# Performance work log

Hardware: AMD Instinct MI355X
Metric: run time of the kernel (lower is better)

Reference implementation:

```python
import jax, jax.numpy as jnp
import numpy as np

N = 13627
E = 504378
D = 500


def _seg_softmax(e, seg, n):
    m = jax.ops.segment_max(e, seg, num_segments=n)
    ex = jnp.exp(e - m[seg])
    s = jax.ops.segment_sum(ex, seg, num_segments=n)
    return ex / (s[seg] + 1e-16)


def _gatv2(x, src, dst, Wl, Wr, att, b, n):
    # PyG GATv2Conv (heads=1): message = Wl x_src; score uses Wl x_src + Wr x_dst
    xl = x @ Wl                                   # [N, F]
    xr = x @ Wr                                   # [N, F]
    e = jax.nn.leaky_relu(xl[src] + xr[dst], 0.2) @ att   # [E]
    a = _seg_softmax(e, dst, n)                   # segment softmax over targets
    out = jax.ops.segment_sum(a[:, None] * xl[src], dst, num_segments=n)
    return out + b


def setup_inputs() -> dict:
    key = jax.random.key(0)
    ks = jax.random.split(key, 24)
    s = 0.05
    inp = {
        'x': jax.random.normal(ks[0], (N, D), dtype=jnp.float32),
        'edge_index': jax.random.randint(ks[1], (2, E), 0, N),
        'neg_edge_index': jax.random.randint(ks[2], (2, E), 0, N),
        'Wl1': jax.random.normal(ks[3], (D, 300)) * s,
        'Wr1': jax.random.normal(ks[4], (D, 300)) * s,
        'att1': jax.random.normal(ks[5], (300,)) * s,
        'b1': jnp.zeros((300,)),
        'Wl2': jax.random.normal(ks[6], (300, 100)) * s,
        'Wr2': jax.random.normal(ks[7], (300, 100)) * s,
        'att2': jax.random.normal(ks[8], (100,)) * s,
        'b2': jnp.zeros((100,)),
        'Wl3': jax.random.normal(ks[9], (100, 1)) * s,
        'Wr3': jax.random.normal(ks[10], (100, 1)) * s,
        'att3': jax.random.normal(ks[11], (1,)) * s,
        'b3': jnp.zeros((1,)),
        'W_lin1': jax.random.normal(ks[12], (D, 100)) * s,
        'b_lin1': jnp.zeros((100,)),
        'W_lin2': jax.random.normal(ks[13], (D, 100)) * s,
        'b_lin2': jnp.zeros((100,)),
        'c1': jnp.array([0.5], dtype=jnp.float32),
        'c2': jnp.array([0.5], dtype=jnp.float32),
    }
    return inp


def reference(x, edge_index, neg_edge_index, Wl1, Wr1, att1, b1, Wl2, Wr2, att2, b2,
              Wl3, Wr3, att3, b3, W_lin1, b_lin1, W_lin2, b_lin2, c1, c2):
    # eval mode: dropout / dropout_adj are identity
    loops = jnp.arange(N)
    src = jnp.concatenate([edge_index[0], loops])   # GATv2Conv adds self loops
    dst = jnp.concatenate([edge_index[1], loops])

    h1 = jax.nn.relu(_gatv2(x, src, dst, Wl1, Wr1, att1, b1, N))
    h2 = jax.nn.relu(_gatv2(h1, src, dst, Wl2, Wr2, att2, b2, N))

    xo = h2 + jax.nn.relu(x @ W_lin1 + b_lin1)
    z = h2 + jax.nn.relu(x @ W_lin2 + b_lin2)

    # link-prediction reconstruction loss
    pos_s = jnp.sum(z[edge_index[0]] * z[edge_index[1]], axis=1)
    pos_loss = -jnp.mean(jnp.log(jax.nn.sigmoid(pos_s) + 1e-15))
    neg_s = jnp.sum(z[neg_edge_index[0]] * z[neg_edge_index[1]], axis=1)
    neg_loss = -jnp.mean(jnp.log(1.0 - jax.nn.sigmoid(neg_s) + 1e-15))
    r_loss = pos_loss + neg_loss

    out = _gatv2(xo, src, dst, Wl3, Wr3, att3, b3, N)   # [N, 1]
    return out, r_loss, c1, c2
```

## Files before the change

### kernel.cpp

```cpp
#include <hip/hip_runtime.h>
#include <hip/hip_bf16.h>

#define NODES 13627
#define DIM   500

typedef short short8 __attribute__((ext_vector_type(8)));
typedef float f32x4 __attribute__((ext_vector_type(4)));
typedef float floatx2 __attribute__((ext_vector_type(2)));

__device__ inline float wave_reduce_sum(float v) {
#pragma unroll
    for (int o = 32; o > 0; o >>= 1) v += __shfl_xor(v, o, 64);
    return v;
}

__device__ inline void store_v(float* p, float v) { *p = v; }
__device__ inline void store_v(__hip_bfloat16* p, float v) { *p = __float2bfloat16(v); }

__device__ inline float blo(unsigned w) { unsigned t = w << 16;        return __builtin_bit_cast(float, t); }
__device__ inline float bhi(unsigned w) { unsigned t = w & 0xffff0000u; return __builtin_bit_cast(float, t); }

__device__ inline unsigned char to_fp8(float v) {
    int r = __builtin_amdgcn_cvt_pk_fp8_f32(v, v, 0, false);
    return (unsigned char)(r & 0xff);
}

__device__ inline unsigned pk2bf(float a, float b) {
    unsigned la = (unsigned)__builtin_bit_cast(unsigned short, __float2bfloat16(a));
    unsigned hb = (unsigned)__builtin_bit_cast(unsigned short, __float2bfloat16(b));
    return la | (hb << 16);
}

struct b4 { __hip_bfloat16 a, b, c, d; };

__global__ __launch_bounds__(256) void hist_kernel(const int* __restrict__ dst,
                                                   int* __restrict__ cnt, int E) {
    int i = blockIdx.x * blockDim.x + threadIdx.x;
    if (i < E) atomicAdd(&cnt[dst[i]], 1);
}

__global__ __launch_bounds__(1024) void scan_kernel(int* __restrict__ cnt_cur,
                                                    int* __restrict__ off, int n) {
    __shared__ int wsum[16];
    const int tid = threadIdx.x, lane = tid & 63, w = tid >> 6;
    int carry = 0;
    for (int base = 0; base < n; base += 1024) {
        int i = base + tid;
        int v = (i < n) ? cnt_cur[i] : 0;
        int s = v;
#pragma unroll
        for (int o = 1; o < 64; o <<= 1) {
            int t = __shfl_up(s, o, 64);
            if (lane >= o) s += t;
        }
        if (lane == 63) wsum[w] = s;
        __syncthreads();
        if (w == 0 && lane < 16) {
            int x = wsum[lane];
            int sx = x;
#pragma unroll
            for (int o = 1; o < 16; o <<= 1) {
                int t = __shfl_up(sx, o, 64);
                if (lane >= o) sx += t;
            }
            wsum[lane] = sx;
        }
        __syncthreads();
        int wo = (w == 0) ? 0 : wsum[w - 1];
        int total = wsum[15];
        int excl = carry + wo + (s - v);
        if (i < n) { off[i] = excl; cnt_cur[i] = excl; }
        carry += total;
        __syncthreads();
    }
    if (tid == 0) off[n] = carry;
}

__global__ __launch_bounds__(256) void scatter_kernel(const int* __restrict__ src,
                                                      const int* __restrict__ dst,
                                                      int* __restrict__ cur,
                                                      int* __restrict__ ssrc, int E) {
    int i = blockIdx.x * blockDim.x + threadIdx.x;
    if (i < E) {
        int p = atomicAdd(&cur[dst[i]], 1);
        ssrc[p] = src[i];
    }
}

__global__ __launch_bounds__(256) void convert_all_kernel(
    const float* __restrict__ x,
    const float* __restrict__ Wl1, const float* __restrict__ Wr1,
    const float* __restrict__ Wl2, const float* __restrict__ Wr2,
    const float* __restrict__ Ws1, const float* __restrict__ Ws2,
    const float* __restrict__ bs1, const float* __restrict__ bs2,
    __hip_bfloat16* __restrict__ W1T, __hip_bfloat16* __restrict__ W2T,
    __hip_bfloat16* __restrict__ WsT, float* __restrict__ bcat,
    __hip_bfloat16* __restrict__ xb, int M) {
    int i = blockIdx.x * 256 + threadIdx.x;
    if (i < 327680) {
        int n = i >> 9, k = i & 511;
        float v = 0.f;
        if (k < 500) {
            if (n < 300) v = Wl1[k * 300 + n];
            else if (n < 600) v = Wr1[k * 300 + n - 300];
        }
        W1T[i] = __float2bfloat16(v);
    } else if (i < 409600) {
        int j = i - 327680;
        int n = j / 320, k = j - n * 320;
        float v = 0.f;
        if (k < 300) {
            if (n < 100) v = Wl2[k * 100 + n];
            else if (n < 200) v = Wr2[k * 100 + n - 100];
        }
        W2T[j] = __float2bfloat16(v);
    } else if (i < 540672) {
        int j = i - 409600;
        int n = j >> 9, k = j & 511;
        float v = 0.f;
        if (k < 500) {
            if (n < 100) v = Ws1[k * 100 + n];
            else if (n < 200) v = Ws2[k * 100 + n - 100];
        }
        WsT[j] = __float2bfloat16(v);
    } else if (i < 540928) {
        int n = i - 540672;
        float v = 0.f;
        if (n < 100) v = bs1[n];
        else if (n < 200) v = bs2[n - 100];
        bcat[n] = v;
    } else {
        int j = i - 540928;
        if (j >= M * 128) return;
        int m = j >> 7, k = (j & 127) << 2;
        b4 o;
        if (k < 500) {
            float4 v = *(const float4*)(x + (size_t)m * 500 + k);
            o.a = __float2bfloat16(v.x); o.b = __float2bfloat16(v.y);
            o.c = __float2bfloat16(v.z); o.d = __float2bfloat16(v.w);
        } else {
            o.a = o.b = o.c = o.d = __float2bfloat16(0.f);
        }
        *(b4*)(xb + (size_t)m * 512 + k) = o;
    }
}

template <int EPI, typename TC>
__global__ __launch_bounds__(256) void mfma_gemm(
    const __hip_bfloat16* __restrict__ A, const __hip_bfloat16* __restrict__ BT,
    TC* __restrict__ C, const float* __restrict__ bias, const float* __restrict__ h2,
    unsigned char* __restrict__ p8, __hip_bfloat16* __restrict__ pb,
    int M, int Kp, int Nn, int ldc) {
    __shared__ short AsF[8 * 64 * 8];
    __shared__ short BsF[4 * 64 * 8];
    const int t = threadIdx.x;
    const int w = t >> 6, lane = t & 63;
    const int c = t & 3, rr = t >> 2;
    const int m0 = blockIdx.y * 128, n0 = blockIdx.x * 64;

    f32x4 acc[2][4];
#pragma unroll
    for (int i = 0; i < 2; i++)
#pragma unroll
        for (int j = 0; j < 4; j++) acc[i][j] = (f32x4){0.f, 0.f, 0.f, 0.f};

    for (int k0 = 0; k0 < Kp; k0 += 32) {
#pragma unroll
        for (int r = 0; r < 2; r++) {
            int m = r * 64 + rr;
            int gm = m0 + m; if (gm >= M) gm = M - 1;
            float4 v = *(const float4*)(A + (size_t)gm * Kp + k0 + c * 8);
            int mi = m >> 4, sl = m & 15;
            *(float4*)(&AsF[(mi * 64 + c * 16 + sl) * 8]) = v;
        }
        {
            int n = rr;
            float4 v = *(const float4*)(BT + (size_t)(n0 + n) * Kp + k0 + c * 8);
            int ni = n >> 4, sl = n & 15;
            *(float4*)(&BsF[(ni * 64 + c * 16 + sl) * 8]) = v;
        }
        __syncthreads();
        short8 a0 = *(const short8*)(&AsF[((w * 2 + 0) * 64 + lane) * 8]);
        short8 a1 = *(const short8*)(&AsF[((w * 2 + 1) * 64 + lane) * 8]);
#pragma unroll
        for (int j = 0; j < 4; j++) {
            short8 b = *(const short8*)(&BsF[(j * 64 + lane) * 8]);
            acc[0][j] = __builtin_amdgcn_mfma_f32_16x16x32_bf16(a0, b, acc[0][j], 0, 0, 0);
            acc[1][j] = __builtin_amdgcn_mfma_f32_16x16x32_bf16(a1, b, acc[1][j], 0, 0, 0);
        }
        __syncthreads();
    }

    const int q = lane >> 4, sl = lane & 15;
#pragma unroll
    for (int i = 0; i < 2; i++) {
#pragma unroll
        for (int j = 0; j < 4; j++) {
#pragma unroll
            for (int reg = 0; reg < 4; reg++) {
                int gm = m0 + w * 32 + i * 16 + q * 4 + reg;
                int gn = n0 + j * 16 + sl;
                if (gm >= M) continue;
                float v = acc[i][j][reg];
                if constexpr (EPI == 1) {
                    if (gn < 300)       p8[(size_t)gm * 304 + gn] = to_fp8(v);
                    else if (gn < 600)  pb[(size_t)gm * 320 + (gn - 300)] = __float2bfloat16(v);
                    else if (gn < 620)  pb[(size_t)gm * 320 + (gn - 300)] = __float2bfloat16(0.f);
                    else if (gn < 624)  p8[(size_t)gm * 304 + (gn - 320)] = 0;
                } else if constexpr (EPI == 2) {
                    if (gn < 100)       p8[(size_t)gm * 112 + gn] = to_fp8(v);
                    else if (gn < 200)  pb[(size_t)gm * 128 + (gn - 100)] = __float2bfloat16(v);
                    else if (gn < 212)  p8[(size_t)gm * 112 + (gn - 100)] = 0;
                    else if (gn < 240)  pb[(size_t)gm * 128 + (gn - 112)] = __float2bfloat16(0.f);
                } else if constexpr (EPI == 3) {
                    if (gn < 200) {
                        int cn = gn < 100 ? gn : gn - 100;
                        float val = fmaxf(v + bias[gn], 0.f) + h2[(size_t)gm * 100 + cn];
                        if (gn < 100) C[(size_t)gm * 100 + gn] = val;
                        else p8[(size_t)gm * 128 + (gn - 100)] = to_fp8(val);
                    } else if (gn < 228) {
                        p8[(size_t)gm * 128 + (gn - 100)] = 0;
                    }
                } else {
                    store_v(&C[(size_t)gm * ldc + gn], v);
                }
            }
        }
    }
}

template <int F, int NJ, int SL8, int SRB, int SOUT, int JSL, typename TOUT>
__global__ __launch_bounds__(256) void gat_f8_kernel(
    const unsigned char* __restrict__ xl8, const __hip_bfloat16* __restrict__ xrb,
    const float* __restrict__ att, const float* __restrict__ bias,
    const int* __restrict__ off, const int* __restrict__ ssrc,
    TOUT* __restrict__ out, int n) {
    __shared__ float sden[2];
    __shared__ float sacc[2][NJ * 64];
    const int t = threadIdx.x;
    const int lane = t & 63;
    const int sl = lane & 15, q = lane >> 4;
    const int half = (t >> 6) & 1;
    const int pairIdx = t >> 7;
    int wid = blockIdx.x * 2 + pairIdx;
    if (wid >= n) wid = n - 1;

    float attv[NJ * 4], xrv[NJ * 4], acc[NJ * 4];
    const unsigned* xru = (const unsigned*)xrb + (size_t)wid * (SRB / 2);
#pragma unroll
    for (int j = 0; j < NJ; j++) {
        const int f0 = sl * 4 + j * 64;
        if (f0 < F) {
            float4 a4 = *(const float4*)(att + f0);
            attv[j * 4 + 0] = a4.x; attv[j * 4 + 1] = a4.y;
            attv[j * 4 + 2] = a4.z; attv[j * 4 + 3] = a4.w;
        } else {
            attv[j * 4 + 0] = attv[j * 4 + 1] = attv[j * 4 + 2] = attv[j * 4 + 3] = 0.f;
        }
        unsigned u0 = __builtin_nontemporal_load(xru + (f0 >> 1));
        unsigned u1 = __builtin_nontemporal_load(xru + (f0 >> 1) + 1);
        xrv[j * 4 + 0] = blo(u0); xrv[j * 4 + 1] = bhi(u0);
        xrv[j * 4 + 2] = blo(u1); xrv[j * 4 + 3] = bhi(u1);
        acc[j * 4 + 0] = acc[j * 4 + 1] = acc[j * 4 + 2] = acc[j * 4 + 3] = 0.f;
    }

    const int s0 = off[wid], s1 = off[wid + 1];
    const int h0 = (s1 - s0) >> 1;
    const int eb = half ? (s0 + h0) : (s0 - 1);
    const int ee = half ? s1 : (s0 + h0);
    float den = 0.f;

    unsigned u[NJ];
    {
        int eq = eb + q;
        int src = wid;
        if (eq >= s0 && eq < ee) src = __builtin_nontemporal_load(ssrc + eq);
        const unsigned char* row = xl8 + (size_t)src * SL8;
#pragma unroll
        for (int j = 0; j < NJ; j++) {
            const bool ld = (j < NJ - 1) || (sl < JSL);
            u[j] = ld ? *(const unsigned*)(row + sl * 4 + j * 64) : 0u;
        }
    }

    for (int e0 = eb; e0 < ee; e0 += 4) {
        const bool act = (e0 + q) < ee;
        unsigned un[NJ];
        {
            int eq1 = e0 + 4 + q;
            int src1 = wid;
            if (eq1 >= s0 && eq1 < ee) src1 = __builtin_nontemporal_load(ssrc + eq1);
            const unsigned char* row1 = xl8 + (size_t)src1 * SL8;
#pragma unroll
            for (int j = 0; j < NJ; j++) {
                const bool ld = (j < NJ - 1) || (sl < JSL);
                un[j] = ld ? *(const unsigned*)(row1 + sl * 4 + j * 64) : 0u;
            }
        }
        float xlv[NJ * 4];
        float p = 0.f;
#pragma unroll
        for (int j = 0; j < NJ; j++) {
            floatx2 lo = __builtin_amdgcn_cvt_pk_f32_fp8((int)u[j], false);
            floatx2 hi = __builtin_amdgcn_cvt_pk_f32_fp8((int)u[j], true);
            float v[4] = {lo.x, lo.y, hi.x, hi.y};
#pragma unroll
            for (int cc = 0; cc < 4; cc++) {
                xlv[j * 4 + cc] = v[cc];
                float s = v[cc] + xrv[j * 4 + cc];
                p += attv[j * 4 + cc] * fmaxf(s, 0.2f * s);
            }
        }
        p += __shfl_xor(p, 1, 64);
        p += __shfl_xor(p, 2, 64);
        p += __shfl_xor(p, 4, 64);
        p += __shfl_xor(p, 8, 64);
        float ex = act ? expf(p) : 0.f;
        den += ex;
#pragma unroll
        for (int i = 0; i < NJ * 4; i++) acc[i] += ex * xlv[i];
#pragma unroll
        for (int j = 0; j < NJ; j++) u[j] = un[j];
    }

#pragma unroll
    for (int o = 16; o <= 32; o <<= 1) {
        den += __shfl_xor(den, o, 64);
#pragma unroll
        for (int i = 0; i < NJ * 4; i++) acc[i] += __shfl_xor(acc[i], o, 64);
    }

    if (half == 1 && lane < 16) {
        if (lane == 0) sden[pairIdx] = den;
#pragma unroll
        for (int j = 0; j < NJ; j++)
            *(float4*)(&sacc[pairIdx][sl * 4 + j * 64]) =
                make_float4(acc[j * 4 + 0], acc[j * 4 + 1], acc[j * 4 + 2], acc[j * 4 + 3]);
    }
    __syncthreads();
    if (half == 0 && lane < 16) {
        den += sden[pairIdx];
        const float inv = 1.f / (den + 1e-16f);
#pragma unroll
        for (int j = 0; j < NJ; j++) {
            const int f0 = sl * 4 + j * 64;
            if (f0 >= SOUT) continue;
            float4 o4 = *(float4*)(&sacc[pairIdx][f0]);
            float vv[4] = {acc[j * 4 + 0] + o4.x, acc[j * 4 + 1] + o4.y,
                           acc[j * 4 + 2] + o4.z, acc[j * 4 + 3] + o4.w};
            float r[4];
#pragma unroll
            for (int cc = 0; cc < 4; cc++) {
                const int f = f0 + cc;
                float v = 0.f;
                if (f < F) v = fmaxf(vv[cc] * inv + bias[f], 0.f);
                r[cc] = v;
            }
            if constexpr (sizeof(TOUT) == 4) {
                *(float4*)((float*)out + (size_t)wid * SOUT + f0) =
                    make_float4(r[0], r[1], r[2], r[3]);
            } else {
                unsigned* op = (unsigned*)out + (size_t)wid * (SOUT / 2) + (f0 >> 1);
                op[0] = pk2bf(r[0], r[1]);
                op[1] = pk2bf(r[2], r[3]);
            }
        }
    }
}

__global__ __launch_bounds__(256) void gemm_vec1_kernel(
    const float* __restrict__ xo, const float* __restrict__ wl,
    const float* __restrict__ wr, float* __restrict__ xl3,
    float* __restrict__ xr3, int M, int ldx) {
    const int wid = blockIdx.x * 4 + (threadIdx.x >> 6);
    const int lane = threadIdx.x & 63;
    if (wid >= M) return;
    float a = 0.f, b = 0.f;
    for (int f = lane; f < 100; f += 64) {
        float v = xo[(size_t)wid * ldx + f];
        a += v * wl[f];
        b += v * wr[f];
    }
    a = wave_reduce_sum(a);
    b = wave_reduce_sum(b);
    if (lane == 0) { xl3[wid] = a; xr3[wid] = b; }
}

__global__ __launch_bounds__(256) void gat3_kernel(
    const float* __restrict__ xl3, const float* __restrict__ xr3,
    const float* __restrict__ att3, const float* __restrict__ b3,
    const int* __restrict__ off, const int* __restrict__ ssrc,
    float* __restrict__ out, int n) {
    const int wid = blockIdx.x * 4 + (threadIdx.x >> 6);
    const int lane = threadIdx.x & 63;
    if (wid >= n) return;
    const float xrv = xr3[wid];
    const float att = att3[0];
    float num = 0.f, den = 0.f;
    const int s0 = off[wid], s1 = off[wid + 1];
    for (int e = s0 - 1 + lane; e < s1; e += 64) {
        int src = (e < s0) ? wid : ssrc[e];
        float xlv = xl3[src];
        float t = xlv + xrv;
        float g = t > 0.f ? t : 0.2f * t;
        float ex = expf(g * att);
        den += ex;
        num += ex * xlv;
    }
    num = wave_reduce_sum(num);
    den = wave_reduce_sum(den);
    if (lane == 0) out[wid] = num / (den + 1e-16f) + b3[0];
}

__global__ __launch_bounds__(256) void loss_kernel(
    const unsigned char* __restrict__ z8, const int* __restrict__ pos,
    const int* __restrict__ neg, float* __restrict__ part, int nb, int E) {
    const int lane = threadIdx.x & 63;
    const int sl = lane & 15;
    const int wlocal = threadIdx.x >> 6;
    const int q = lane >> 4;
    const int nq = gridDim.x * 16;
    const int qid = (blockIdx.x * 4 + wlocal) * 4 + q;
    const int total = 2 * E;
    float psum = 0.f, nsum = 0.f;

    for (int base = qid; base < total; base += 4 * nq) {
        uint2 au[4], bu[4];
        bool act[4], isN[4];
#pragma unroll
        for (int s = 0; s < 4; s++) {
            int it = base + s * nq;
            act[s] = it < total;
            int itc = act[s] ? it : 0;
            isN[s] = itc >= E;
            int e = isN[s] ? itc - E : itc;
            const int* ei = isN[s] ? neg : pos;
            int u = ei[e], v = ei[E + e];
            au[s] = *(const uint2*)(z8 + (size_t)u * 128 + sl * 8);
            bu[s] = *(const uint2*)(z8 + (size_t)v * 128 + sl * 8);
        }
#pragma unroll
        for (int s = 0; s < 4; s++) {
            floatx2 a0 = __builtin_amdgcn_cvt_pk_f32_fp8((int)au[s].x, false);
            floatx2 a1 = __builtin_amdgcn_cvt_pk_f32_fp8((int)au[s].x, true);
            floatx2 a2 = __builtin_amdgcn_cvt_pk_f32_fp8((int)au[s].y, false);
            floatx2 a3 = __builtin_amdgcn_cvt_pk_f32_fp8((int)au[s].y, true);
            floatx2 b0 = __builtin_amdgcn_cvt_pk_f32_fp8((int)bu[s].x, false);
            floatx2 b1 = __builtin_amdgcn_cvt_pk_f32_fp8((int)bu[s].x, true);
            floatx2 b2 = __builtin_amdgcn_cvt_pk_f32_fp8((int)bu[s].y, false);
            floatx2 b3 = __builtin_amdgcn_cvt_pk_f32_fp8((int)bu[s].y, true);
            float p = a0.x * b0.x + a0.y * b0.y + a1.x * b1.x + a1.y * b1.y
                    + a2.x * b2.x + a2.y * b2.y + a3.x * b3.x + a3.y * b3.y;
            p += __shfl_xor(p, 1, 64);
            p += __shfl_xor(p, 2, 64);
            p += __shfl_xor(p, 4, 64);
            p += __shfl_xor(p, 8, 64);
            if (sl == 0 && act[s]) {
                float sig = 1.f / (1.f + expf(-p));
                if (isN[s]) nsum += logf(1.f - sig + 1e-15f);
                else        psum += logf(sig + 1e-15f);
            }
        }
    }
    float pw = wave_reduce_sum(psum);
    float nw = wave_reduce_sum(nsum);
    __shared__ float sp[4], sn[4];
    if (lane == 0) { sp[wlocal] = pw; sn[wlocal] = nw; }
    __syncthreads();
    if (threadIdx.x == 0) {
        part[blockIdx.x]      = sp[0] + sp[1] + sp[2] + sp[3];
        part[nb + blockIdx.x] = sn[0] + sn[1] + sn[2] + sn[3];
    }
}

__global__ __launch_bounds__(1024) void finalize_kernel(
    const float* __restrict__ part, int nb,
    const float* __restrict__ c1, const float* __restrict__ c2,
    float* __restrict__ out, int n, int E) {
    __shared__ float sp[16], sn[16];
    const int tid = threadIdx.x, lane = tid & 63, w = tid >> 6;
    float p = 0.f, q = 0.f;
    for (int i = tid; i < nb; i += 1024) { p += part[i]; q += part[nb + i]; }
    p = wave_reduce_sum(p);
    q = wave_reduce_sum(q);
    if (lane == 0) { sp[w] = p; sn[w] = q; }
    __syncthreads();
    if (tid == 0) {
        float tp = 0.f, tq = 0.f;
#pragma unroll
        for (int i = 0; i < 16; i++) { tp += sp[i]; tq += sn[i]; }
        out[n]     = -(tp + tq) / (float)E;
        out[n + 1] = c1[0];
        out[n + 2] = c2[0];
    }
}

extern "C" void kernel_launch(void* const* d_in, const int* in_sizes, int n_in,
                              void* d_out, int out_size, void* d_ws, size_t ws_size,
                              hipStream_t stream) {
    const float* x      = (const float*)d_in[0];
    const int*   ei     = (const int*)d_in[1];
    const int*   nei    = (const int*)d_in[2];
    const float* Wl1    = (const float*)d_in[3];
    const float* Wr1    = (const float*)d_in[4];
    const float* att1   = (const float*)d_in[5];
    const float* b1     = (const float*)d_in[6];
    const float* Wl2    = (const float*)d_in[7];
    const float* Wr2    = (const float*)d_in[8];
    const float* att2   = (const float*)d_in[9];
    const float* b2     = (const float*)d_in[10];
    const float* Wl3    = (const float*)d_in[11];
    const float* Wr3    = (const float*)d_in[12];
    const float* att3   = (const float*)d_in[13];
    const float* b3     = (const float*)d_in[14];
    const float* Wlin1  = (const float*)d_in[15];
    const float* blin1  = (const float*)d_in[16];
    const float* Wlin2  = (const float*)d_in[17];
    const float* blin2  = (const float*)d_in[18];
    const float* c1     = (const float*)d_in[19];
    const float* c2     = (const float*)d_in[20];
    float* out = (float*)d_out;

    const int E = in_sizes[1] / 2;
    const int N = NODES;
    const int LOSS_BLOCKS = 4096;

    char* ws = (char*)d_ws;
    unsigned char*  xl8  = (unsigned char*)(ws + 0);
    unsigned char*  xl28 = (unsigned char*)(ws + 0);
    __hip_bfloat16* xrb  = (__hip_bfloat16*)(ws + 4194304);
    __hip_bfloat16* xr2b = (__hip_bfloat16*)(ws + 4194304);
    float*          xo   = (float*)(ws + 4194304);
    unsigned char*  z8   = (unsigned char*)(ws + 9645312);
    __hip_bfloat16* h1b  = (__hip_bfloat16*)(ws + 12915712);
    float*          h2   = (float*)(ws + 12915712);
    __hip_bfloat16* xb   = (__hip_bfloat16*)(ws + 21637120);
    __hip_bfloat16* W1T  = (__hip_bfloat16*)(ws + 35591168);
    __hip_bfloat16* W2T  = (__hip_bfloat16*)(ws + 36246528);
    __hip_bfloat16* WsT  = (__hip_bfloat16*)(ws + 36410368);
    float*          bcat = (float*)(ws + 36672512);
    float*          xl3  = (float*)(ws + 36673536);
    float*          xr3  = (float*)(ws + 36728064);
    int*            ioff = (int*)(ws + 36782592);
    int*            cur  = (int*)(ws + 36837376);
    int*            ssrc = (int*)(ws + 36892160);
    float*          part = (float*)(ws + 38909952);

    hipMemsetAsync(cur, 0, sizeof(int) * N, stream);

    hist_kernel<<<(E + 255) / 256, 256, 0, stream>>>(ei + E, cur, E);
    scan_kernel<<<1, 1024, 0, stream>>>(cur, ioff, N);
    scatter_kernel<<<(E + 255) / 256, 256, 0, stream>>>(ei, ei + E, cur, ssrc, E);

    convert_all_kernel<<<(540928 + N * 128 + 255) / 256, 256, 0, stream>>>(
        x, Wl1, Wr1, Wl2, Wr2, Wlin1, Wlin2, blin1, blin2,
        W1T, W2T, WsT, bcat, xb, N);

    mfma_gemm<1, __hip_bfloat16><<<dim3(10, 107), 256, 0, stream>>>(
        xb, W1T, (__hip_bfloat16*)nullptr, nullptr, nullptr, xl8, xrb, N, 512, 640, 0);
    gat_f8_kernel<300, 5, 304, 320, 320, 11, __hip_bfloat16>
        <<<(N + 1) / 2, 256, 0, stream>>>(xl8, xrb, att1, b1, ioff, ssrc, h1b, N);

    mfma_gemm<2, __hip_bfloat16><<<dim3(4, 107), 256, 0, stream>>>(
        h1b, W2T, (__hip_bfloat16*)nullptr, nullptr, nullptr, xl28, xr2b, N, 320, 256, 0);
    gat_f8_kernel<100, 2, 112, 128, 100, 9, float>
        <<<(N + 1) / 2, 256, 0, stream>>>(xl28, xr2b, att2, b2, ioff, ssrc, h2, N);

    mfma_gemm<3, float><<<dim3(4, 107), 256, 0, stream>>>(
        xb, WsT, xo, bcat, h2, z8, nullptr, N, 512, 256, 0);

    loss_kernel<<<LOSS_BLOCKS, 256, 0, stream>>>(z8, ei, nei, part, LOSS_BLOCKS, E);

    gemm_vec1_kernel<<<(N + 3) / 4, 256, 0, stream>>>(xo, Wl3, Wr3, xl3, xr3, N, 100);
    gat3_kernel<<<(N + 3) / 4, 256, 0, stream>>>(xl3, xr3, att3, b3, ioff, ssrc, out, N);

    finalize_kernel<<<1, 1024, 0, stream>>>(part, LOSS_BLOCKS, c1, c2, out, N, E);
}
```

Baseline: 390.4 us.

## Split leaky-ReLU into linear plus abs terms, precompute linear part in GEMM epilogue

Rewrites leaky_relu(s) as 0.6*s + 0.4*|s|, so the linear term att·(xl_src + xr_dst) is computed once per node in the GEMM epilogue via shuffle reductions and atomics into per-node scalars. The edge loop then only does an fma with |s| and adds the two precomputed scalars, replacing a max and multiply per feature. In exchange it adds atomics and reductions to the GEMM epilogue, an extra memset, and a per-edge scalar gather. The linear term now comes from fp32 accumulators rather than the fp8-quantized xl values, which slightly changes the numerics.

```diff
diff --git a/kernel.cpp b/kernel.cpp
--- a/kernel.cpp
+++ b/kernel.cpp
@@ -150,6 +150,7 @@
     const __hip_bfloat16* __restrict__ A, const __hip_bfloat16* __restrict__ BT,
     TC* __restrict__ C, const float* __restrict__ bias, const float* __restrict__ h2,
     unsigned char* __restrict__ p8, __hip_bfloat16* __restrict__ pb,
+    const float* __restrict__ attw, float* __restrict__ sxl, float* __restrict__ sxr,
     int M, int Kp, int Nn, int ldc) {
     __shared__ short AsF[8 * 64 * 8];
     __shared__ short BsF[4 * 64 * 8];
@@ -192,37 +193,75 @@
     }
 
     const int q = lane >> 4, sl = lane & 15;
-#pragma unroll
-    for (int i = 0; i < 2; i++) {
-#pragma unroll
-        for (int j = 0; j < 4; j++) {
+    if constexpr (EPI == 1 || EPI == 2) {
+        constexpr int XL_END = (EPI == 1) ? 300 : 100;
+        constexpr int XR_END = 2 * XL_END;
+        constexpr int SL8s   = (EPI == 1) ? 304 : 112;
+        constexpr int SRBs   = (EPI == 1) ? 320 : 128;
+        const bool hasXl = n0 < XL_END;
+        const bool hasXr = (n0 + 63 >= XL_END) && (n0 < XR_END);
+#pragma unroll
+        for (int i = 0; i < 2; i++) {
 #pragma unroll
             for (int reg = 0; reg < 4; reg++) {
                 int gm = m0 + w * 32 + i * 16 + q * 4 + reg;
-                int gn = n0 + j * 16 + sl;
                 if (gm >= M) continue;
-                float v = acc[i][j][reg];
-                if constexpr (EPI == 1) {
-                    if (gn < 300)       p8[(size_t)gm * 304 + gn] = to_fp8(v);
-                    else if (gn < 600)  pb[(size_t)gm * 320 + (gn - 300)] = __float2bfloat16(v);
-                    else if (gn < 620)  pb[(size_t)gm * 320 + (gn - 300)] = __float2bfloat16(0.f);
-                    else if (gn < 624)  p8[(size_t)gm * 304 + (gn - 320)] = 0;
-                } else if constexpr (EPI == 2) {
-                    if (gn < 100)       p8[(size_t)gm * 112 + gn] = to_fp8(v);
-                    else if (gn < 200)  pb[(size_t)gm * 128 + (gn - 100)] = __float2bfloat16(v);
-                    else if (gn < 212)  p8[(size_t)gm * 112 + (gn - 100)] = 0;
-                    else if (gn < 240)  pb[(size_t)gm * 128 + (gn - 112)] = __float2bfloat16(0.f);
-                } else if constexpr (EPI == 3) {
-                    if (gn < 200) {
-                        int cn = gn < 100 ? gn : gn - 100;
-                        float val = fmaxf(v + bias[gn], 0.f) + h2[(size_t)gm * 100 + cn];
-                        if (gn < 100) C[(size_t)gm * 100 + gn] = val;
-                        else p8[(size_t)gm * 128 + (gn - 100)] = to_fp8(val);
-                    } else if (gn < 228) {
-                        p8[(size_t)gm * 128 + (gn - 100)] = 0;
+                float axl = 0.f, axr = 0.f;
+#pragma unroll
+                for (int j = 0; j < 4; j++) {
+                    int gn = n0 + j * 16 + sl;
+                    float v = acc[i][j][reg];
+                    if (gn < XL_END) {
+                        p8[(size_t)gm * SL8s + gn] = to_fp8(v);
+                        axl += attw[gn] * v;
+                    } else if (gn < XR_END) {
+                        pb[(size_t)gm * SRBs + (gn - XL_END)] = __float2bfloat16(v);
+                        axr += attw[gn - XL_END] * v;
+                    } else {
+                        if constexpr (EPI == 1) {
+                            if (gn < 620)      pb[(size_t)gm * 320 + (gn - 300)] = __float2bfloat16(0.f);
+                            else if (gn < 624) p8[(size_t)gm * 304 + (gn - 320)] = 0;
+                        } else {
+                            if (gn < 212)      p8[(size_t)gm * 112 + (gn - 100)] = 0;
+                            else if (gn < 240) pb[(size_t)gm * 128 + (gn - 112)] = __float2bfloat16(0.f);
+                        }
                     }
-                } else {
-                    store_v(&C[(size_t)gm * ldc + gn], v);
+                }
+                if (hasXl) {
+#pragma unroll
+                    for (int o = 1; o < 16; o <<= 1) axl += __shfl_xor(axl, o, 64);
+                    if (sl == 0) atomicAdd(&sxl[gm], 0.6f * axl);
+                }
+                if (hasXr) {
+#pragma unroll
+                    for (int o = 1; o < 16; o <<= 1) axr += __shfl_xor(axr, o, 64);
+                    if (sl == 0) atomicAdd(&sxr[gm], 0.6f * axr);
+                }
+            }
+        }
+    } else {
+#pragma unroll
+        for (int i = 0; i < 2; i++) {
+#pragma unroll
+            for (int j = 0; j < 4; j++) {
+#pragma unroll
+                for (int reg = 0; reg < 4; reg++) {
+                    int gm = m0 + w * 32 + i * 16 + q * 4 + reg;
+                    int gn = n0 + j * 16 + sl;
+                    if (gm >= M) continue;
+                    float v = acc[i][j][reg];
+                    if constexpr (EPI == 3) {
+                        if (gn < 200) {
+                            int cn = gn < 100 ? gn : gn - 100;
+                            float val = fmaxf(v + bias[gn], 0.f) + h2[(size_t)gm * 100 + cn];
+                            if (gn < 100) C[(size_t)gm * 100 + gn] = val;
+                            else p8[(size_t)gm * 128 + (gn - 100)] = to_fp8(val);
+                        } else if (gn < 228) {
+                            p8[(size_t)gm * 128 + (gn - 100)] = 0;
+                        }
+                    } else {
+                        store_v(&C[(size_t)gm * ldc + gn], v);
+                    }
                 }
             }
         }
@@ -233,6 +272,7 @@
 __global__ __launch_bounds__(256) void gat_f8_kernel(
     const unsigned char* __restrict__ xl8, const __hip_bfloat16* __restrict__ xrb,
     const float* __restrict__ att, const float* __restrict__ bias,
+    const float* __restrict__ sxl, const float* __restrict__ sxr,
     const int* __restrict__ off, const int* __restrict__ ssrc,
     TOUT* __restrict__ out, int n) {
     __shared__ float sden[2];
@@ -245,17 +285,17 @@
     int wid = blockIdx.x * 2 + pairIdx;
     if (wid >= n) wid = n - 1;
 
-    float attv[NJ * 4], xrv[NJ * 4], acc[NJ * 4];
+    float att4[NJ * 4], xrv[NJ * 4], acc[NJ * 4];
     const unsigned* xru = (const unsigned*)xrb + (size_t)wid * (SRB / 2);
 #pragma unroll
     for (int j = 0; j < NJ; j++) {
         const int f0 = sl * 4 + j * 64;
         if (f0 < F) {
             float4 a4 = *(const float4*)(att + f0);
-            attv[j * 4 + 0] = a4.x; attv[j * 4 + 1] = a4.y;
-            attv[j * 4 + 2] = a4.z; attv[j * 4 + 3] = a4.w;
+            att4[j * 4 + 0] = 0.4f * a4.x; att4[j * 4 + 1] = 0.4f * a4.y;
+            att4[j * 4 + 2] = 0.4f * a4.z; att4[j * 4 + 3] = 0.4f * a4.w;
         } else {
-            attv[j * 4 + 0] = attv[j * 4 + 1] = attv[j * 4 + 2] = attv[j * 4 + 3] = 0.f;
+            att4[j * 4 + 0] = att4[j * 4 + 1] = att4[j * 4 + 2] = att4[j * 4 + 3] = 0.f;
         }
         unsigned u0 = __builtin_nontemporal_load(xru + (f0 >> 1));
         unsigned u1 = __builtin_nontemporal_load(xru + (f0 >> 1) + 1);
@@ -263,6 +303,7 @@
         xrv[j * 4 + 2] = blo(u1); xrv[j * 4 + 3] = bhi(u1);
         acc[j * 4 + 0] = acc[j * 4 + 1] = acc[j * 4 + 2] = acc[j * 4 + 3] = 0.f;
     }
+    const float pbase = sxr[wid];
 
     const int s0 = off[wid], s1 = off[wid + 1];
     const int h0 = (s1 - s0) >> 1;
@@ -271,6 +312,7 @@
     float den = 0.f;
 
     unsigned u[NJ];
+    float sx;
     {
         int eq = eb + q;
         int src = wid;
@@ -281,11 +323,13 @@
             const bool ld = (j < NJ - 1) || (sl < JSL);
             u[j] = ld ? *(const unsigned*)(row + sl * 4 + j * 64) : 0u;
         }
+        sx = sxl[src];
     }
 
     for (int e0 = eb; e0 < ee; e0 += 4) {
         const bool act = (e0 + q) < ee;
         unsigned un[NJ];
+        float sxn;
         {
             int eq1 = e0 + 4 + q;
             int src1 = wid;
@@ -296,9 +340,10 @@
                 const bool ld = (j < NJ - 1) || (sl < JSL);
                 un[j] = ld ? *(const unsigned*)(row1 + sl * 4 + j * 64) : 0u;
             }
+            sxn = sxl[src1];
         }
         float xlv[NJ * 4];
-        float p = 0.f;
+        float p = (sl == 0) ? (pbase + sx) : 0.f;
 #pragma unroll
         for (int j = 0; j < NJ; j++) {
             floatx2 lo = __builtin_amdgcn_cvt_pk_f32_fp8((int)u[j], false);
@@ -308,7 +353,7 @@
             for (int cc = 0; cc < 4; cc++) {
                 xlv[j * 4 + cc] = v[cc];
                 float s = v[cc] + xrv[j * 4 + cc];
-                p += attv[j * 4 + cc] * fmaxf(s, 0.2f * s);
+                p = fmaf(att4[j * 4 + cc], fabsf(s), p);
             }
         }
         p += __shfl_xor(p, 1, 64);
@@ -321,6 +366,7 @@
         for (int i = 0; i < NJ * 4; i++) acc[i] += ex * xlv[i];
 #pragma unroll
         for (int j = 0; j < NJ; j++) u[j] = un[j];
+        sx = sxn;
     }
 
 #pragma unroll
@@ -545,8 +591,13 @@
     int*            cur  = (int*)(ws + 36837376);
     int*            ssrc = (int*)(ws + 36892160);
     float*          part = (float*)(ws + 38909952);
+    float*          sxl1 = (float*)(ws + 38942720);
+    float*          sxr1 = (float*)(ws + 38997248);
+    float*          sxl2 = (float*)(ws + 39051776);
+    float*          sxr2 = (float*)(ws + 39106304);
 
     hipMemsetAsync(cur, 0, sizeof(int) * N, stream);
+    hipMemsetAsync(sxl1, 0, sizeof(float) * 4 * 54527, stream);
 
     hist_kernel<<<(E + 255) / 256, 256, 0, stream>>>(ei + E, cur, E);
     scan_kernel<<<1, 1024, 0, stream>>>(cur, ioff, N);
@@ -557,17 +608,19 @@
         W1T, W2T, WsT, bcat, xb, N);
 
     mfma_gemm<1, __hip_bfloat16><<<dim3(10, 107), 256, 0, stream>>>(
-        xb, W1T, (__hip_bfloat16*)nullptr, nullptr, nullptr, xl8, xrb, N, 512, 640, 0);
+        xb, W1T, (__hip_bfloat16*)nullptr, nullptr, nullptr, xl8, xrb,
+        att1, sxl1, sxr1, N, 512, 640, 0);
     gat_f8_kernel<300, 5, 304, 320, 320, 11, __hip_bfloat16>
-        <<<(N + 1) / 2, 256, 0, stream>>>(xl8, xrb, att1, b1, ioff, ssrc, h1b, N);
+        <<<(N + 1) / 2, 256, 0, stream>>>(xl8, xrb, att1, b1, sxl1, sxr1, ioff, ssrc, h1b, N);
 
     mfma_gemm<2, __hip_bfloat16><<<dim3(4, 107), 256, 0, stream>>>(
-        h1b, W2T, (__hip_bfloat16*)nullptr, nullptr, nullptr, xl28, xr2b, N, 320, 256, 0);
+        h1b, W2T, (__hip_bfloat16*)nullptr, nullptr, nullptr, xl28, xr2b,
+        att2, sxl2, sxr2, N, 320, 256, 0);
     gat_f8_kernel<100, 2, 112, 128, 100, 9, float>
-        <<<(N + 1) / 2, 256, 0, stream>>>(xl28, xr2b, att2, b2, ioff, ssrc, h2, N);
+        <<<(N + 1) / 2, 256, 0, stream>>>(xl28, xr2b, att2, b2, sxl2, sxr2, ioff, ssrc, h2, N);
 
     mfma_gemm<3, float><<<dim3(4, 107), 256, 0, stream>>>(
-        xb, WsT, xo, bcat, h2, z8, nullptr, N, 512, 256, 0);
+        xb, WsT, xo, bcat, h2, z8, nullptr, nullptr, nullptr, nullptr, N, 512, 256, 0);
 
     loss_kernel<<<LOSS_BLOCKS, 256, 0, stream>>>(z8, ei, nei, part, LOSS_BLOCKS, E);
 
```

Measured after the change: 415.4 us. 1.06x slower.
